# Optimization experiments

Hardware: AMD Instinct MI355X
Metric: run time of the kernel (lower is better)

Reference implementation:

```python
import jax, jax.numpy as jnp
import numpy as np

IN_FEATURES = 4096
OUT_FEATURES = 11008
PACK = 8  # int4 values per int32


def setup_inputs() -> dict:
    key = jax.random.key(0)
    k1, k2, k3, k4, k5 = jax.random.split(key, 5)
    x = jax.random.normal(k1, (1, IN_FEATURES), dtype=jnp.float32)
    # packed int4 weights: 8 nibbles per int32 word, [in/8, out]
    qweight = jax.random.randint(k2, (IN_FEATURES // PACK, OUT_FEATURES), 0, 2147483647, dtype=jnp.int32)
    # per-output-channel quant params; zeros is already zeros*scales (as in __init__)
    scales = jax.random.uniform(k3, (OUT_FEATURES,), jnp.float32, minval=0.005, maxval=0.02)
    zeros = jax.random.uniform(k4, (OUT_FEATURES,), jnp.float32, minval=0.0, maxval=0.16)
    bias = jax.random.normal(k5, (OUT_FEATURES,), dtype=jnp.float32) * 0.01
    return {"x": x, "qweight": qweight, "scales": scales, "zeros": zeros, "bias": bias}


def reference(x, qweight, scales, zeros, bias):
    # unpack 8 int4 nibbles per int32 word along the input dim
    shifts = (jnp.arange(PACK, dtype=jnp.int32) * 4)  # [8]
    q = (qweight[:, None, :] >> shifts[None, :, None]) & 0xF  # [in/8, 8, out]
    q = q.reshape(-1, qweight.shape[-1]).astype(x.dtype)       # [in, out]
    # y = x @ (q*scales - zeros) + bias, factored so the fp matvec hits q directly:
    # scales/zeros are per-output-channel so they distribute out of the contraction.
    xq = x @ q                                                 # [1, out]
    x_sum = jnp.sum(x, axis=-1, keepdims=True)                 # [1, 1]
    return xq * scales - x_sum * zeros + bias                  # [1, out]
```

## Files before the change

### kernel.cpp

```cpp
#include <hip/hip_runtime.h>

#define IN_FEATURES 4096
#define OUT_FEATURES 11008
#define KW (IN_FEATURES / 8)
#define SPLIT 4
#define KWB (KW / SPLIT)
#define BLOCK 256
#define OPB 32
#define KG 32
#define W (KWB / KG)
#define NWAVE (BLOCK / 64)

__global__ __launch_bounds__(BLOCK) void quant4_matvec_split(
    const float* __restrict__ x,
    const int* __restrict__ qw,
    const float* __restrict__ scales,
    const float* __restrict__ zeros,
    const float* __restrict__ bias,
    float* __restrict__ out)
{
    __shared__ float xs[KWB * 8];
    __shared__ float red[NWAVE][OPB];
    __shared__ float xsum_s[NWAVE];

    const int tid = threadIdx.x;
    const int ob  = blockIdx.x;
    const int q   = blockIdx.y;

    const float4* x4 = (const float4*)x;
    float4 v = x4[q * (KWB * 2) + tid];
    ((float4*)xs)[tid] = v;
    float xpart = v.x + v.y + v.z + v.w;
#pragma unroll
    for (int off = 32; off > 0; off >>= 1)
        xpart += __shfl_down(xpart, off);
    if ((tid & 63) == 0) xsum_s[tid >> 6] = xpart;
    __syncthreads();

    const int og = tid & 7;
    const int kg = tid >> 3;
    const int o4 = ob * OPB + og * 4;

    float acc0 = 0.f, acc1 = 0.f, acc2 = 0.f, acc3 = 0.f;
#pragma unroll
    for (int w = 0; w < W; ++w) {
        const int kl = w * KG + kg;
        const int krow = q * KWB + kl;
        const int4 qv = *(const int4*)(qw + (long)krow * OUT_FEATURES + o4);
        const float4 xa = *(const float4*)(&xs[kl * 8]);
        const float4 xb = *(const float4*)(&xs[kl * 8 + 4]);
        const float xv[8] = {xa.x, xa.y, xa.z, xa.w, xb.x, xb.y, xb.z, xb.w};
        const unsigned qx = (unsigned)qv.x, qy = (unsigned)qv.y,
                       qz = (unsigned)qv.z, qwv = (unsigned)qv.w;
#pragma unroll
        for (int n = 0; n < 8; ++n) {
            const float xvn = xv[n];
            acc0 += xvn * (float)((qx >> (4 * n)) & 0xFu);
            acc1 += xvn * (float)((qy >> (4 * n)) & 0xFu);
            acc2 += xvn * (float)((qz >> (4 * n)) & 0xFu);
            acc3 += xvn * (float)((qwv >> (4 * n)) & 0xFu);
        }
    }

#pragma unroll
    for (int m = 8; m <= 32; m <<= 1) {
        acc0 += __shfl_xor(acc0, m);
        acc1 += __shfl_xor(acc1, m);
        acc2 += __shfl_xor(acc2, m);
        acc3 += __shfl_xor(acc3, m);
    }
    const int lane = tid & 63;
    const int wid  = tid >> 6;
    if (lane < 8) {
        red[wid][lane * 4 + 0] = acc0;
        red[wid][lane * 4 + 1] = acc1;
        red[wid][lane * 4 + 2] = acc2;
        red[wid][lane * 4 + 3] = acc3;
    }
    __syncthreads();

    if (tid < OPB) {
        float s = 0.f;
#pragma unroll
        for (int g = 0; g < NWAVE; ++g) s += red[g][tid];
        float xsumq = 0.f;
#pragma unroll
        for (int g = 0; g < NWAVE; ++g) xsumq += xsum_s[g];
        const int o = ob * OPB + tid;
        float val = s * scales[o] - xsumq * zeros[o];
        if (q == 0) val += bias[o];
        atomicAdd(out + o, val);
    }
}

extern "C" void kernel_launch(void* const* d_in, const int* in_sizes, int n_in,
                              void* d_out, int out_size, void* d_ws, size_t ws_size,
                              hipStream_t stream) {
    const float* x      = (const float*)d_in[0];
    const int*   qw     = (const int*)d_in[1];
    const float* scales = (const float*)d_in[2];
    const float* zeros  = (const float*)d_in[3];
    const float* bias   = (const float*)d_in[4];
    float* out = (float*)d_out;

    hipMemsetAsync(out, 0, OUT_FEATURES * sizeof(float), stream);

    dim3 grid(OUT_FEATURES / OPB, SPLIT);
    quant4_matvec_split<<<grid, BLOCK, 0, stream>>>(x, qw, scales, zeros, bias, out);
}
```

Baseline: 80.12 us.

## Replace memset with init kernel and restructure matvec for wide coalesced loads

A small init kernel now computes the x-sum and writes bias minus xsum*zeros into the output, replacing the memset. The main kernel uses 128-output tiles with an 8-way K split, and each thread issues 8 independent int4 weight loads up front to raise memory-level parallelism. Each warp-row reads a contiguous 512B span, and x is read straight from global memory instead of shared. The cross-wave shared reduction and syncthreads are gone; partials go to global atomics after a single xor shuffle. The cost is more atomics (8 K-splits times 8 row groups per output) and an extra kernel launch.

```diff
diff --git a/kernel.cpp b/kernel.cpp
--- a/kernel.cpp
+++ b/kernel.cpp
@@ -3,93 +3,89 @@
 #define IN_FEATURES 4096
 #define OUT_FEATURES 11008
 #define KW (IN_FEATURES / 8)
-#define SPLIT 4
-#define KWB (KW / SPLIT)
+#define OTILE 128
+#define NOTILE (OUT_FEATURES / OTILE)
+#define KSPLIT 8
+#define ROWS_B (KW / KSPLIT)
 #define BLOCK 256
-#define OPB 32
-#define KG 32
-#define W (KWB / KG)
-#define NWAVE (BLOCK / 64)
+#define W 8
 
-__global__ __launch_bounds__(BLOCK) void quant4_matvec_split(
+__global__ __launch_bounds__(BLOCK) void q4_init(
     const float* __restrict__ x,
-    const int* __restrict__ qw,
-    const float* __restrict__ scales,
     const float* __restrict__ zeros,
     const float* __restrict__ bias,
     float* __restrict__ out)
 {
-    __shared__ float xs[KWB * 8];
-    __shared__ float red[NWAVE][OPB];
-    __shared__ float xsum_s[NWAVE];
+    __shared__ float part[BLOCK / 64];
+    const int tid = threadIdx.x;
+    const float4* x4 = (const float4*)x;
 
-    const int tid = threadIdx.x;
-    const int ob  = blockIdx.x;
-    const int q   = blockIdx.y;
+    float s = 0.f;
+#pragma unroll
+    for (int i = 0; i < (IN_FEATURES / 4) / BLOCK; ++i) {
+        const float4 v = x4[i * BLOCK + tid];
+        s += (v.x + v.y) + (v.z + v.w);
+    }
+#pragma unroll
+    for (int off = 32; off > 0; off >>= 1) s += __shfl_down(s, off);
+    if ((tid & 63) == 0) part[tid >> 6] = s;
+    __syncthreads();
+    const float xsum = (part[0] + part[1]) + (part[2] + part[3]);
+
+    const int o = blockIdx.x * BLOCK + tid;
+    out[o] = bias[o] - xsum * zeros[o];
+}
+
+__global__ __launch_bounds__(BLOCK) void q4_main(
+    const float* __restrict__ x,
+    const int* __restrict__ qw,
+    const float* __restrict__ scales,
+    float* __restrict__ out)
+{
+    const int tid  = threadIdx.x;
+    const int og   = tid & 31;
+    const int half = (tid >> 5) & 1;
+    const int wv   = tid >> 6;
+
+    const int o4 = blockIdx.x * OTILE + og * 4;
+    const int r0 = blockIdx.y * ROWS_B + wv * 16 + half * 8;
+
+    const int* qp = qw + (long)r0 * OUT_FEATURES + o4;
+    int4 qv[W];
+#pragma unroll
+    for (int i = 0; i < W; ++i)
+        qv[i] = *(const int4*)(qp + (long)i * OUT_FEATURES);
 
     const float4* x4 = (const float4*)x;
-    float4 v = x4[q * (KWB * 2) + tid];
-    ((float4*)xs)[tid] = v;
-    float xpart = v.x + v.y + v.z + v.w;
-#pragma unroll
-    for (int off = 32; off > 0; off >>= 1)
-        xpart += __shfl_down(xpart, off);
-    if ((tid & 63) == 0) xsum_s[tid >> 6] = xpart;
-    __syncthreads();
-
-    const int og = tid & 7;
-    const int kg = tid >> 3;
-    const int o4 = ob * OPB + og * 4;
-
     float acc0 = 0.f, acc1 = 0.f, acc2 = 0.f, acc3 = 0.f;
 #pragma unroll
-    for (int w = 0; w < W; ++w) {
-        const int kl = w * KG + kg;
-        const int krow = q * KWB + kl;
-        const int4 qv = *(const int4*)(qw + (long)krow * OUT_FEATURES + o4);
-        const float4 xa = *(const float4*)(&xs[kl * 8]);
-        const float4 xb = *(const float4*)(&xs[kl * 8 + 4]);
+    for (int i = 0; i < W; ++i) {
+        const float4 xa = x4[(r0 + i) * 2 + 0];
+        const float4 xb = x4[(r0 + i) * 2 + 1];
         const float xv[8] = {xa.x, xa.y, xa.z, xa.w, xb.x, xb.y, xb.z, xb.w};
-        const unsigned qx = (unsigned)qv.x, qy = (unsigned)qv.y,
-                       qz = (unsigned)qv.z, qwv = (unsigned)qv.w;
+        const unsigned qx = (unsigned)qv[i].x, qy = (unsigned)qv[i].y,
+                       qz = (unsigned)qv[i].z, qt = (unsigned)qv[i].w;
 #pragma unroll
         for (int n = 0; n < 8; ++n) {
             const float xvn = xv[n];
             acc0 += xvn * (float)((qx >> (4 * n)) & 0xFu);
             acc1 += xvn * (float)((qy >> (4 * n)) & 0xFu);
             acc2 += xvn * (float)((qz >> (4 * n)) & 0xFu);
-            acc3 += xvn * (float)((qwv >> (4 * n)) & 0xFu);
+            acc3 += xvn * (float)((qt >> (4 * n)) & 0xFu);
         }
     }
 
-#pragma unroll
-    for (int m = 8; m <= 32; m <<= 1) {
-        acc0 += __shfl_xor(acc0, m);
-        acc1 += __shfl_xor(acc1, m);
-        acc2 += __shfl_xor(acc2, m);
-        acc3 += __shfl_xor(acc3, m);
-    }
-    const int lane = tid & 63;
-    const int wid  = tid >> 6;
-    if (lane < 8) {
-        red[wid][lane * 4 + 0] = acc0;
-        red[wid][lane * 4 + 1] = acc1;
-        red[wid][lane * 4 + 2] = acc2;
-        red[wid][lane * 4 + 3] = acc3;
-    }
-    __syncthreads();
+    acc0 += __shfl_xor(acc0, 32);
+    acc1 += __shfl_xor(acc1, 32);
+    acc2 += __shfl_xor(acc2, 32);
+    acc3 += __shfl_xor(acc3, 32);
 
-    if (tid < OPB) {
-        float s = 0.f;
-#pragma unroll
-        for (int g = 0; g < NWAVE; ++g) s += red[g][tid];
-        float xsumq = 0.f;
-#pragma unroll
-        for (int g = 0; g < NWAVE; ++g) xsumq += xsum_s[g];
-        const int o = ob * OPB + tid;
-        float val = s * scales[o] - xsumq * zeros[o];
-        if (q == 0) val += bias[o];
-        atomicAdd(out + o, val);
+    if ((tid & 32) == 0) {
+        const float4 sc = *(const float4*)(scales + o4);
+        atomicAdd(out + o4 + 0, acc0 * sc.x);
+        atomicAdd(out + o4 + 1, acc1 * sc.y);
+        atomicAdd(out + o4 + 2, acc2 * sc.z);
+        atomicAdd(out + o4 + 3, acc3 * sc.w);
     }
 }
 
@@ -103,8 +99,6 @@
     const float* bias   = (const float*)d_in[4];
     float* out = (float*)d_out;
 
-    hipMemsetAsync(out, 0, OUT_FEATURES * sizeof(float), stream);
-
-    dim3 grid(OUT_FEATURES / OPB, SPLIT);
-    quant4_matvec_split<<<grid, BLOCK, 0, stream>>>(x, qw, scales, zeros, bias, out);
+    q4_init<<<dim3(OUT_FEATURES / BLOCK), BLOCK, 0, stream>>>(x, zeros, bias, out);
+    q4_main<<<dim3(NOTILE, KSPLIT), BLOCK, 0, stream>>>(x, qw, scales, out);
 }
```

Result: slower. 84.47 us (+5.4%).

## Drop split-K atomics; preload all weight tiles into registers per block

Applied to the files above, without the earlier changes.

Replaces the 4-way split-K grid (memset plus atomicAdd) with one 512-thread block per 32-output tile that covers the full K dimension. Each thread issues all of its int4 weight loads up front into a register array, so many memory requests are in flight at once. x is read straight from global memory instead of being staged in LDS, and the nibbles are extracted with paired 0x0F0F0F0F masks. This removes the memset launch and the atomics, but the register array raises register pressure and the grid has fewer blocks.

```diff
diff --git a/kernel.cpp b/kernel.cpp
--- a/kernel.cpp
+++ b/kernel.cpp
@@ -3,15 +3,14 @@
 #define IN_FEATURES 4096
 #define OUT_FEATURES 11008
 #define KW (IN_FEATURES / 8)
-#define SPLIT 4
-#define KWB (KW / SPLIT)
-#define BLOCK 256
-#define OPB 32
-#define KG 32
-#define W (KWB / KG)
+#define OTILE 32
+#define NBLK (OUT_FEATURES / OTILE)
+#define BLOCK 512
 #define NWAVE (BLOCK / 64)
+#define KGROUPS (BLOCK / 8)
+#define W (KW / KGROUPS)
 
-__global__ __launch_bounds__(BLOCK) void quant4_matvec_split(
+__global__ __launch_bounds__(BLOCK) void q4_matvec(
     const float* __restrict__ x,
     const int* __restrict__ qw,
     const float* __restrict__ scales,
@@ -19,47 +18,66 @@
     const float* __restrict__ bias,
     float* __restrict__ out)
 {
-    __shared__ float xs[KWB * 8];
-    __shared__ float red[NWAVE][OPB];
-    __shared__ float xsum_s[NWAVE];
+    __shared__ float red[NWAVE][OTILE];
+    __shared__ float xred[NWAVE];
 
     const int tid = threadIdx.x;
-    const int ob  = blockIdx.x;
-    const int q   = blockIdx.y;
+    const int og  = tid & 7;
+    const int kg  = tid >> 3;
+    const int o4  = blockIdx.x * OTILE + og * 4;
+
+    const int* qp = qw + (long)kg * OUT_FEATURES + o4;
+    int4 qv[W];
+#pragma unroll
+    for (int i = 0; i < W; ++i)
+        qv[i] = *(const int4*)(qp + (long)i * KGROUPS * OUT_FEATURES);
 
     const float4* x4 = (const float4*)x;
-    float4 v = x4[q * (KWB * 2) + tid];
-    ((float4*)xs)[tid] = v;
-    float xpart = v.x + v.y + v.z + v.w;
-#pragma unroll
-    for (int off = 32; off > 0; off >>= 1)
-        xpart += __shfl_down(xpart, off);
-    if ((tid & 63) == 0) xsum_s[tid >> 6] = xpart;
-    __syncthreads();
-
-    const int og = tid & 7;
-    const int kg = tid >> 3;
-    const int o4 = ob * OPB + og * 4;
-
     float acc0 = 0.f, acc1 = 0.f, acc2 = 0.f, acc3 = 0.f;
 #pragma unroll
-    for (int w = 0; w < W; ++w) {
-        const int kl = w * KG + kg;
-        const int krow = q * KWB + kl;
-        const int4 qv = *(const int4*)(qw + (long)krow * OUT_FEATURES + o4);
-        const float4 xa = *(const float4*)(&xs[kl * 8]);
-        const float4 xb = *(const float4*)(&xs[kl * 8 + 4]);
-        const float xv[8] = {xa.x, xa.y, xa.z, xa.w, xb.x, xb.y, xb.z, xb.w};
-        const unsigned qx = (unsigned)qv.x, qy = (unsigned)qv.y,
-                       qz = (unsigned)qv.z, qwv = (unsigned)qv.w;
-#pragma unroll
-        for (int n = 0; n < 8; ++n) {
-            const float xvn = xv[n];
-            acc0 += xvn * (float)((qx >> (4 * n)) & 0xFu);
-            acc1 += xvn * (float)((qy >> (4 * n)) & 0xFu);
-            acc2 += xvn * (float)((qz >> (4 * n)) & 0xFu);
-            acc3 += xvn * (float)((qwv >> (4 * n)) & 0xFu);
-        }
+    for (int i = 0; i < W; ++i) {
+        const int r = kg + i * KGROUPS;
+        const float4 xa = x4[r * 2 + 0];
+        const float4 xb = x4[r * 2 + 1];
+        const unsigned q0 = (unsigned)qv[i].x, q1 = (unsigned)qv[i].y,
+                       q2 = (unsigned)qv[i].z, q3 = (unsigned)qv[i].w;
+
+        {   const unsigned e = q0 & 0x0F0F0F0Fu, o = (q0 >> 4) & 0x0F0F0F0Fu;
+            acc0 += xa.x * (float)(e & 0xFFu);
+            acc0 += xa.y * (float)(o & 0xFFu);
+            acc0 += xa.z * (float)((e >> 8) & 0xFFu);
+            acc0 += xa.w * (float)((o >> 8) & 0xFFu);
+            acc0 += xb.x * (float)((e >> 16) & 0xFFu);
+            acc0 += xb.y * (float)((o >> 16) & 0xFFu);
+            acc0 += xb.z * (float)((e >> 24) & 0xFFu);
+            acc0 += xb.w * (float)(o >> 24); }
+        {   const unsigned e = q1 & 0x0F0F0F0Fu, o = (q1 >> 4) & 0x0F0F0F0Fu;
+            acc1 += xa.x * (float)(e & 0xFFu);
+            acc1 += xa.y * (float)(o & 0xFFu);
+            acc1 += xa.z * (float)((e >> 8) & 0xFFu);
+            acc1 += xa.w * (float)((o >> 8) & 0xFFu);
+            acc1 += xb.x * (float)((e >> 16) & 0xFFu);
+            acc1 += xb.y * (float)((o >> 16) & 0xFFu);
+            acc1 += xb.z * (float)((e >> 24) & 0xFFu);
+            acc1 += xb.w * (float)(o >> 24); }
+        {   const unsigned e = q2 & 0x0F0F0F0Fu, o = (q2 >> 4) & 0x0F0F0F0Fu;
+            acc2 += xa.x * (float)(e & 0xFFu);
+            acc2 += xa.y * (float)(o & 0xFFu);
+            acc2 += xa.z * (float)((e >> 8) & 0xFFu);
+            acc2 += xa.w * (float)((o >> 8) & 0xFFu);
+            acc2 += xb.x * (float)((e >> 16) & 0xFFu);
+            acc2 += xb.y * (float)((o >> 16) & 0xFFu);
+            acc2 += xb.z * (float)((e >> 24) & 0xFFu);
+            acc2 += xb.w * (float)(o >> 24); }
+        {   const unsigned e = q3 & 0x0F0F0F0Fu, o = (q3 >> 4) & 0x0F0F0F0Fu;
+            acc3 += xa.x * (float)(e & 0xFFu);
+            acc3 += xa.y * (float)(o & 0xFFu);
+            acc3 += xa.z * (float)((e >> 8) & 0xFFu);
+            acc3 += xa.w * (float)((o >> 8) & 0xFFu);
+            acc3 += xb.x * (float)((e >> 16) & 0xFFu);
+            acc3 += xb.y * (float)((o >> 16) & 0xFFu);
+            acc3 += xb.z * (float)((e >> 24) & 0xFFu);
+            acc3 += xb.w * (float)(o >> 24); }
     }
 
 #pragma unroll
@@ -77,19 +95,26 @@
         red[wid][lane * 4 + 2] = acc2;
         red[wid][lane * 4 + 3] = acc3;
     }
+
+    {
+        const float4 a = x4[tid];
+        const float4 b = x4[tid + BLOCK];
+        float xs = (a.x + a.y + a.z + a.w) + (b.x + b.y + b.z + b.w);
+#pragma unroll
+        for (int off = 32; off > 0; off >>= 1) xs += __shfl_down(xs, off);
+        if (lane == 0) xred[wid] = xs;
+    }
     __syncthreads();
 
-    if (tid < OPB) {
+    if (tid < OTILE) {
         float s = 0.f;
 #pragma unroll
         for (int g = 0; g < NWAVE; ++g) s += red[g][tid];
-        float xsumq = 0.f;
+        float xsum = 0.f;
 #pragma unroll
-        for (int g = 0; g < NWAVE; ++g) xsumq += xsum_s[g];
-        const int o = ob * OPB + tid;
-        float val = s * scales[o] - xsumq * zeros[o];
-        if (q == 0) val += bias[o];
-        atomicAdd(out + o, val);
+        for (int g = 0; g < NWAVE; ++g) xsum += xred[g];
+        const int o = blockIdx.x * OTILE + tid;
+        out[o] = s * scales[o] - xsum * zeros[o] + bias[o];
     }
 }
 
@@ -103,8 +128,5 @@
     const float* bias   = (const float*)d_in[4];
     float* out = (float*)d_out;
 
-    hipMemsetAsync(out, 0, OUT_FEATURES * sizeof(float), stream);
-
-    dim3 grid(OUT_FEATURES / OPB, SPLIT);
-    quant4_matvec_split<<<grid, BLOCK, 0, stream>>>(x, qw, scales, zeros, bias, out);
+    q4_matvec<<<dim3(NBLK), BLOCK, 0, stream>>>(x, qw, scales, zeros, bias, out);
 }
```

After: 80.26 us. About the same (+0.2%).
